# Kernel optimization log

Hardware: AMD Instinct MI355X
Metric: run time of the kernel (lower is better)

## Reference

```python
import jax, jax.numpy as jnp
import numpy as np

H = 4096        # hidden_size
I = 11008       # intermediate_size
R = 32          # low-rank error-correction rank
NLEV = 16       # int4 -> 16 levels
Q_ZERO = 7.5    # symmetric int4 zero point
Q_STEP = 0.005  # per-channel scale multiplier (keeps dequantized weights ~N(0, 1/sqrt(H)) scale)
LR_SCALE = 0.02 # low-rank correction magnitude


def setup_inputs() -> dict:
    key = jax.random.key(0)
    ks = jax.random.split(key, 13)
    B, S = 2, 2048
    inp = {
        "x": jax.random.normal(ks[0], (B, S, H), jnp.float32),
        "gate_q": jax.random.randint(ks[1], (I, H), 0, NLEV, jnp.int32),
        "gate_scale": jax.random.uniform(ks[2], (I,), jnp.float32),
        "gate_A": jax.random.normal(ks[3], (H, R), jnp.float32),
        "gate_B": jax.random.normal(ks[4], (R, I), jnp.float32),
        "up_q": jax.random.randint(ks[5], (I, H), 0, NLEV, jnp.int32),
        "up_scale": jax.random.uniform(ks[6], (I,), jnp.float32),
        "up_A": jax.random.normal(ks[7], (H, R), jnp.float32),
        "up_B": jax.random.normal(ks[8], (R, I), jnp.float32),
        "down_q": jax.random.randint(ks[9], (H, I), 0, NLEV, jnp.int32),
        "down_scale": jax.random.uniform(ks[10], (H,), jnp.float32),
        "down_A": jax.random.normal(ks[11], (I, R), jnp.float32),
        "down_B": jax.random.normal(ks[12], (R, H), jnp.float32),
    }
    return inp


def _qlinear(x, q, scale, A, Bm):
    # Dequantize int4 weight [out, in] with per-output-channel scale, then
    # y = x @ W^T + LR_SCALE * (x @ A) @ B   (LQER low-rank error correction)
    w = (q.astype(jnp.float32) - Q_ZERO) * (scale * Q_STEP)[:, None]
    y = jnp.einsum('bsh,oh->bso', x, w)
    return y + LR_SCALE * ((x @ A) @ Bm)


def reference(x, gate_q, gate_scale, gate_A, gate_B,
              up_q, up_scale, up_A, up_B,
              down_q, down_scale, down_A, down_B):
    g = _qlinear(x, gate_q, gate_scale, gate_A, gate_B)   # [B,S,I]
    u = _qlinear(x, up_q, up_scale, up_A, up_B)           # [B,S,I]
    h = jax.nn.silu(g) * u                                # SwiGLU gating
    return _qlinear(h, down_q, down_scale, down_A, down_B)  # [B,S,H]
```

## Files before the change

kernel.cpp:

```cpp
#include <hip/hip_runtime.h>
#include <hip/hip_bf16.h>
#include <stdint.h>

#define H_DIM 4096
#define I_DIM 11008
#define M_TOK 4096

typedef __attribute__((ext_vector_type(8))) short short8;
typedef __attribute__((ext_vector_type(4))) float f32x4;
typedef __attribute__((ext_vector_type(4))) int   i32x4;

#define SX_DIV 6.0f
#define QS (0.0025f * SX_DIV / 127.0f)

static __device__ __forceinline__ float bf2f(unsigned short u) {
    union { uint32_t i; float f; } v; v.i = ((uint32_t)u) << 16; return v.f;
}
static __device__ __forceinline__ unsigned short f2bf(float f) {
    union { float f; uint32_t i; } v; v.f = f;
    uint32_t r = v.i + 0x7FFF + ((v.i >> 16) & 1);
    return (unsigned short)(r >> 16);
}

static __device__ __forceinline__ void gload16(const void* g, void* l) {
    __builtin_amdgcn_global_load_lds(
        (const __attribute__((address_space(1))) void*)g,
        (__attribute__((address_space(3))) void*)l, 16, 0, 0);
}

__global__ void k_prep_all(
    const float* __restrict__ x,
    const int* __restrict__ gq, const int* __restrict__ uq,
    const float* __restrict__ gA, const float* __restrict__ uA,
    const float* __restrict__ dA,
    const float* __restrict__ gB, const float* __restrict__ uB,
    const float* __restrict__ dB,
    unsigned short* __restrict__ xbf, char* __restrict__ xi8,
    char* __restrict__ Wg8, char* __restrict__ Wu8,
    unsigned short* __restrict__ AgT, unsigned short* __restrict__ AuT,
    unsigned short* __restrict__ AdBf,
    unsigned short* __restrict__ BgT, unsigned short* __restrict__ BuT,
    unsigned short* __restrict__ BdT)
{
    const int stride = gridDim.x * blockDim.x;
    const int tid0 = blockIdx.x * blockDim.x + threadIdx.x;
    const int XN4 = (M_TOK * H_DIM) / 4;
    const float SXI = 127.0f / SX_DIV;
    for (int i = tid0; i < XN4; i += stride) {
        f32x4 v = ((const f32x4*)x)[i];
        uint64_t p = (uint64_t)f2bf(v[0]) | ((uint64_t)f2bf(v[1]) << 16) |
                     ((uint64_t)f2bf(v[2]) << 32) | ((uint64_t)f2bf(v[3]) << 48);
        ((uint64_t*)xbf)[i] = p;
        uint32_t q8 = 0;
#pragma unroll
        for (int t = 0; t < 4; t++) {
            int a = (int)lrintf(v[t] * SXI);
            a = a > 127 ? 127 : (a < -127 ? -127 : a);
            q8 |= ((uint32_t)(a & 255)) << (8 * t);
        }
        ((uint32_t*)xi8)[i] = q8;
    }
    const int QN4 = (I_DIM * H_DIM) / 4;
    for (int i = tid0; i < 2 * QN4; i += stride) {
        int j = i; const int* src; char* dst;
        if (j < QN4) { src = gq; dst = Wg8; } else { j -= QN4; src = uq; dst = Wu8; }
        i32x4 qv = ((const i32x4*)src)[j];
        uint32_t p = 0;
#pragma unroll
        for (int t = 0; t < 4; t++)
            p |= ((uint32_t)((2 * qv[t] - 15) & 255)) << (8 * t);
        ((uint32_t*)dst)[j] = p;
    }
    const int AT = 32 * H_DIM;
    for (int i = tid0; i < 2 * AT; i += stride) {
        int j = i; const float* src; unsigned short* dst;
        if (j < AT) { src = gA; dst = AgT; } else { j -= AT; src = uA; dst = AuT; }
        int r = j >> 12, k = j & 4095;
        dst[j] = f2bf(src[k * 32 + r]);
    }
    const int AD = I_DIM * 32;
    for (int i = tid0; i < AD; i += stride) AdBf[i] = f2bf(dA[i]);
    const int TBI = I_DIM * 32, TBH = H_DIM * 32;
    for (int i = tid0; i < 2 * TBI + TBH; i += stride) {
        int j = i; const float* src; unsigned short* dst; int N;
        if (j < TBI) { src = gB; dst = BgT; N = I_DIM; }
        else if ((j -= TBI) < TBI) { src = uB; dst = BuT; N = I_DIM; }
        else { j -= TBI; src = dB; dst = BdT; N = H_DIM; }
        int n = j >> 5, r = j & 31;
        dst[j] = f2bf(src[r * N + n]);
    }
}

__global__ __launch_bounds__(256) void k_T(
    const unsigned short* __restrict__ xbf,
    const unsigned short* __restrict__ AgT,
    const unsigned short* __restrict__ AuT,
    unsigned short* __restrict__ Tg,
    unsigned short* __restrict__ Tu)
{
    const unsigned short* AT = blockIdx.y ? AuT : AgT;
    unsigned short* T = blockIdx.y ? Tu : Tg;
    const int wid = threadIdx.x >> 6, lane = threadIdx.x & 63;
    const int base = blockIdx.x * 64 + wid * 16;
    const int l15 = lane & 15, kg = (lane >> 4) * 8;
    f32x4 acc0 = {}, acc1 = {};
    for (int k0 = 0; k0 < H_DIM; k0 += 32) {
        short8 af = *(const short8*)&xbf[(size_t)(base + l15) * H_DIM + k0 + kg];
        short8 b0 = *(const short8*)&AT[(size_t)l15 * H_DIM + k0 + kg];
        short8 b1 = *(const short8*)&AT[(size_t)(16 + l15) * H_DIM + k0 + kg];
        acc0 = __builtin_amdgcn_mfma_f32_16x16x32_bf16(af, b0, acc0, 0, 0, 0);
        acc1 = __builtin_amdgcn_mfma_f32_16x16x32_bf16(af, b1, acc1, 0, 0, 0);
    }
    const int q4 = lane >> 4;
#pragma unroll
    for (int t = 0; t < 4; t++) {
        int m = base + q4 * 4 + t;
        T[m * 32 + l15]      = f2bf(acc0[t] * 0.02f);
        T[m * 32 + 16 + l15] = f2bf(acc1[t] * 0.02f);
    }
}

__global__ __launch_bounds__(256) void k_wprep(
    const unsigned short* __restrict__ BT,
    const unsigned short* __restrict__ Abf,
    const int* __restrict__ q,
    const float* __restrict__ scale,
    unsigned short* __restrict__ W,
    int Nw, int Kw)
{
    __shared__ unsigned short As[128 * 32];
    __shared__ unsigned short Bs[128 * 32];
    const int tid = threadIdx.x, wid = tid >> 6, lane = tid & 63;
    const int wr = wid >> 1, wc = wid & 1;
    const int brow = blockIdx.y * 128;
    const int bcol = blockIdx.x * 128;
    const int srow = wid * 16 + (lane >> 2), scol = (lane & 3) * 8;

    gload16(BT + (size_t)(brow + srow) * 32 + scol,        &As[wid * 512]);
    gload16(BT + (size_t)(brow + 64 + srow) * 32 + scol,   &As[wid * 512 + 2048]);
    gload16(Abf + (size_t)(bcol + srow) * 32 + scol,       &Bs[wid * 512]);
    gload16(Abf + (size_t)(bcol + 64 + srow) * 32 + scol,  &Bs[wid * 512 + 2048]);
    __syncthreads();

    const int fr = lane & 15, kg = (lane >> 4) * 8;
    f32x4 acc[4][4] = {};
    short8 af[4], bfr[4];
#pragma unroll
    for (int i = 0; i < 4; i++)
        af[i] = *(const short8*)&As[(wr * 64 + i * 16 + fr) * 32 + kg];
#pragma unroll
    for (int j = 0; j < 4; j++)
        bfr[j] = *(const short8*)&Bs[(wc * 64 + j * 16 + fr) * 32 + kg];
#pragma unroll
    for (int i = 0; i < 4; i++)
#pragma unroll
        for (int j = 0; j < 4; j++)
            acc[i][j] = __builtin_amdgcn_mfma_f32_16x16x32_bf16(af[i], bfr[j], acc[i][j], 0, 0, 0);

    const int q4 = lane >> 4;
#pragma unroll
    for (int i = 0; i < 4; i++) {
#pragma unroll
        for (int t = 0; t < 4; t++) {
            int n = brow + wr * 64 + i * 16 + q4 * 4 + t;
            float sc = scale[n] * 0.005f;
#pragma unroll
            for (int j = 0; j < 4; j++) {
                int k = bcol + wc * 64 + j * 16 + fr;
                size_t off = (size_t)n * Kw + k;
                float w = ((float)q[off] - 7.5f) * sc + 0.02f * acc[i][j][t];
                W[off] = f2bf(w);
            }
        }
    }
}

__global__ __launch_bounds__(512, 1) void k_gemmfu8(
    const char* __restrict__ Xq,
    const char* __restrict__ Wg8,
    const char* __restrict__ Wu8,
    const unsigned short* __restrict__ Tg,
    const unsigned short* __restrict__ Tu,
    const unsigned short* __restrict__ BgT,
    const unsigned short* __restrict__ BuT,
    const float* __restrict__ gs, const float* __restrict__ us,
    unsigned short* __restrict__ H,
    int M, int NI, int K)
{
    extern __shared__ char dynsmem[];
    char* smem = dynsmem;
    const int tid = threadIdx.x, wid = tid >> 6, lane = tid & 63;
    const int wr = wid >> 2, wc = wid & 3;

    const int gx = NI >> 7;
    const int nwg = gx * (M >> 8);
    int orig = blockIdx.y * gx + blockIdx.x;
    int q8 = nwg >> 3, r8 = nwg & 7;
    int xcd = orig & 7, lid = orig >> 3;
    int wg = (xcd < r8 ? xcd * (q8 + 1) : r8 * (q8 + 1) + (xcd - r8) * q8) + lid;
    const int bcol = (wg % gx) << 7;
    const int brow = (wg / gx) << 8;

    const int srow = wid * 16 + (lane >> 2);
    const int scolB = ((lane & 3) ^ ((lane >> 3) & 3)) * 16;
    const char* aSrc  = Xq  + (size_t)(brow + srow) * K + scolB;
    const char* bgSrc = Wg8 + (size_t)(bcol + srow) * K + scolB;
    const char* buSrc = Wu8 + (size_t)(bcol + srow) * K + scolB;
    const int ldwB = wid * 1024;

    i32x4 acc[8][4];
#pragma unroll
    for (int i = 0; i < 8; ++i)
#pragma unroll
        for (int j = 0; j < 4; ++j) acc[i][j] = (i32x4){0, 0, 0, 0};

    i32x4 A0f[4], A1f[4], BgAf[2], BgBf[2], Buf[2];
    const int l15 = lane & 15, q4b = lane >> 4;
    const int ps = (q4b ^ ((l15 >> 1) & 3)) * 16;
    const char* aRd = smem + (wr * 64 + l15) * 64 + ps;
    const char* bRd = smem + 16384 + (wc * 32 + l15) * 64 + ps;
    const int NT = K >> 6;

#define SA0(BB, k0) gload16(aSrc + (k0), smem + (BB)*32768 + ldwB)
#define SA1(BB, k0) gload16(aSrc + 128*(size_t)K + (k0), smem + (BB)*32768 + 8192 + ldwB)
#define SBG(BB, k0) gload16(bgSrc + (k0), smem + (BB)*32768 + 16384 + ldwB)
#define SBU(BB, k0) gload16(buSrc + (k0), smem + (BB)*32768 + 24576 + ldwB)
#define LDA0(BB) { _Pragma("unroll") for (int i4 = 0; i4 < 4; ++i4) \
    A0f[i4] = *(const i32x4*)(aRd + (BB)*32768 + i4*1024); }
#define LDA1(BB) { _Pragma("unroll") for (int i4 = 0; i4 < 4; ++i4) \
    A1f[i4] = *(const i32x4*)(aRd + (BB)*32768 + 8192 + i4*1024); }
#define LDBG(SET, BB) { _Pragma("unroll") for (int j2 = 0; j2 < 2; ++j2) \
    SET[j2] = *(const i32x4*)(bRd + (BB)*32768 + j2*1024); }
#define LDBU(BB) { _Pragma("unroll") for (int j2 = 0; j2 < 2; ++j2) \
    Buf[j2] = *(const i32x4*)(bRd + (BB)*32768 + 8192 + j2*1024); }
#define MFI(AF, BF, IH, JB) { __builtin_amdgcn_s_setprio(1); \
    _Pragma("unroll") for (int i4 = 0; i4 < 4; ++i4) \
    _Pragma("unroll") for (int j2 = 0; j2 < 2; ++j2) \
        acc[(IH)*4+i4][(JB)*2+j2] = __builtin_amdgcn_mfma_i32_16x16x64_i8( \
            AF[i4], BF[j2], acc[(IH)*4+i4][(JB)*2+j2], 0, 0, 0); \
    __builtin_amdgcn_s_setprio(0); }
#define BARR() __builtin_amdgcn_s_barrier()

#define FTILE(BB, BGC, BGN, k2, S2, CERT, RN) { \
    LDBU(BB); \
    BARR(); \
    MFI(A0f, BGC, 0, 0); \
    LDA1(BB); \
    BARR(); \
    if (S2) { SA0(BB, k2); SBG(BB, k2); } \
    MFI(A0f, Buf, 0, 1); \
    if (CERT == 1) asm volatile("s_waitcnt vmcnt(2)" ::: "memory"); \
    if (CERT == 2) asm volatile("s_waitcnt vmcnt(0)" ::: "memory"); \
    BARR(); \
    if (S2) { SBU(BB, k2); } \
    MFI(A1f, Buf, 1, 1); \
    if (RN) { LDA0(1-(BB)); LDBG(BGN, 1-(BB)); } \
    BARR(); \
    if (S2) { SA1(BB, k2); } \
    MFI(A1f, BGC, 1, 0); \
}

    SA0(0, 0); SBG(0, 0); SBU(0, 0); SA1(0, 0);
    SA0(1, 64); SBG(1, 64); SBU(1, 64); SA1(1, 64);
    asm volatile("s_waitcnt vmcnt(4)" ::: "memory");
    BARR();
    LDA0(0); LDBG(BgAf, 0);

    for (int u = 0; u < (NT - 2) / 2; ++u) {
        const int k2a = (2 * u + 2) << 6, k2b = (2 * u + 3) << 6;
        FTILE(0, BgAf, BgBf, k2a, 1, 1, 1);
        FTILE(1, BgBf, BgAf, k2b, 1, 1, 1);
    }
    FTILE(0, BgAf, BgBf, 0, 0, 2, 1);
    FTILE(1, BgBf, BgAf, 0, 0, 0, 0);

#undef FTILE
#undef BARR
#undef MFI
#undef LDBU
#undef LDBG
#undef LDA1
#undef LDA0
#undef SBU
#undef SBG
#undef SA1
#undef SA0

    __builtin_amdgcn_s_barrier();
    {
        const int scolH = (lane & 3) * 8;
        gload16(Tg + (size_t)(brow + srow) * 32 + scolH,        smem + ldwB);
        gload16(Tg + (size_t)(brow + 128 + srow) * 32 + scolH,  smem + 8192 + ldwB);
        gload16(Tu + (size_t)(brow + srow) * 32 + scolH,        smem + 16384 + ldwB);
        gload16(Tu + (size_t)(brow + 128 + srow) * 32 + scolH,  smem + 24576 + ldwB);
        gload16(BgT + (size_t)(bcol + srow) * 32 + scolH,       smem + 32768 + ldwB);
        gload16(BuT + (size_t)(bcol + srow) * 32 + scolH,       smem + 40960 + ldwB);
    }
    asm volatile("s_waitcnt vmcnt(0)" ::: "memory");
    __builtin_amdgcn_s_barrier();

    const int fr = l15;
    short8 BgF[2], BuF[2];
#pragma unroll
    for (int j2 = 0; j2 < 2; ++j2) {
        BgF[j2] = *(const short8*)(smem + 32768 + (wc * 32 + j2 * 16 + l15) * 64 + q4b * 16);
        BuF[j2] = *(const short8*)(smem + 40960 + (wc * 32 + j2 * 16 + l15) * 64 + q4b * 16);
    }
    float cg[2], cu[2];
#pragma unroll
    for (int j2 = 0; j2 < 2; ++j2) {
        int n = bcol + wc * 32 + j2 * 16 + fr;
        cg[j2] = gs[n] * QS;
        cu[j2] = us[n] * QS;
    }
    const int q4 = lane >> 4;
#pragma unroll
    for (int i = 0; i < 8; ++i) {
        int trow = (i >> 2) * 128 + wr * 64 + (i & 3) * 16 + l15;
        short8 tgf = *(const short8*)(smem + trow * 64 + q4b * 16);
        short8 tuf = *(const short8*)(smem + 16384 + trow * 64 + q4b * 16);
#pragma unroll
        for (int j2 = 0; j2 < 2; ++j2) {
            f32x4 ag, au;
#pragma unroll
            for (int t = 0; t < 4; ++t) {
                ag[t] = (float)acc[i][j2][t] * cg[j2];
                au[t] = (float)acc[i][2 + j2][t] * cu[j2];
            }
            ag = __builtin_amdgcn_mfma_f32_16x16x32_bf16(tgf, BgF[j2], ag, 0, 0, 0);
            au = __builtin_amdgcn_mfma_f32_16x16x32_bf16(tuf, BuF[j2], au, 0, 0, 0);
#pragma unroll
            for (int t = 0; t < 4; ++t) {
                int m = brow + (i >> 2) * 128 + wr * 64 + (i & 3) * 16 + q4 * 4 + t;
                int n = bcol + wc * 32 + j2 * 16 + fr;
                float g = ag[t];
                float s = g / (1.0f + __expf(-g));
                H[(size_t)m * NI + n] = f2bf(s * au[t]);
            }
        }
    }
}

#define STG(p, k0, doff) gload16((p) + (k0), smem + (doff) + ldw)
#define LDA8(dst, P, IH) { _Pragma("unroll") \
    for (int i4 = 0; i4 < 4; ++i4) dst[i4] = *(const short8*)&(P)[(IH)*8192 + i4*1024]; }
#define LDB4(dst, P, JH) { _Pragma("unroll") \
    for (int j2 = 0; j2 < 2; ++j2) dst[j2] = *(const short8*)&(P)[(JH)*8192 + j2*1024]; }
#define MF8(AF, BF, IH, JH) { __builtin_amdgcn_s_setprio(1); \
    _Pragma("unroll") for (int i4 = 0; i4 < 4; ++i4) \
    _Pragma("unroll") for (int j2 = 0; j2 < 2; ++j2) \
        acc[(IH)*4+i4][(JH)*2+j2] = __builtin_amdgcn_mfma_f32_16x16x32_bf16( \
            AF[i4], BF[j2], acc[(IH)*4+i4][(JH)*2+j2], 0, 0, 0); \
    __builtin_amdgcn_s_setprio(0); }

#define TILE(BB, t, S2, SB0, CERT, RNEXT) { \
    const int kN = ((t) + 1) << 6, kN2 = ((t) + 2) << 6; \
    LDA8(afY, aP[BB][1], 0); LDB4(bfY, bP[BB][1], 0); \
    __builtin_amdgcn_s_barrier(); \
    if (SB0) { STG(bS[0], kN, (1-(BB))*32768 + 16384); \
               STG(bS[1], kN, (1-(BB))*32768 + 20480); } \
    MF8(afX, bfX, 0, 0); \
    LDB4(bfX, bP[BB][0], 1); \
    __builtin_amdgcn_s_barrier(); \
    MF8(afY, bfY, 0, 0); \
    LDB4(bfY, bP[BB][1], 1); \
    __builtin_amdgcn_s_barrier(); \
    if (S2) { STG(aS[0], kN2, (BB)*32768); STG(aS[1], kN2, (BB)*32768 + 4096); } \
    MF8(afX, bfX, 0, 1); \
    LDA8(afX, aP[BB][0], 1); \
    __builtin_amdgcn_s_barrier(); \
    MF8(afY, bfY, 0, 1); \
    LDA8(afY, aP[BB][1], 1); \
    if (CERT == 1) asm volatile("s_waitcnt vmcnt(2)" ::: "memory"); \
    if (CERT == 2) asm volatile("s_waitcnt vmcnt(0)" ::: "memory"); \
    __builtin_amdgcn_s_barrier(); \
    if (S2) { STG(bS[2], kN2, (BB)*32768 + 24576); STG(bS[3], kN2, (BB)*32768 + 28672); } \
    MF8(afX, bfX, 1, 1); \
    LDB4(bfX, bP[BB][0], 0); \
    __builtin_amdgcn_s_barrier(); \
    MF8(afY, bfY, 1, 1); \
    LDB4(bfY, bP[BB][1], 0); \
    __builtin_amdgcn_s_barrier(); \
    if (S2) { STG(aS[2], kN2, (BB)*32768 + 8192); STG(aS[3], kN2, (BB)*32768 + 12288); } \
    MF8(afX, bfX, 1, 0); \
    if (RNEXT) { LDA8(afX, aP[1-(BB)][0], 0); LDB4(bfX, bP[1-(BB)][0], 0); } \
    __builtin_amdgcn_s_barrier(); \
    MF8(afY, bfY, 1, 0); \
}

#define GEMM_BODY(K_) { \
    const int NT = (K_) >> 6; \
    STG(aS[0], 0, 0);      STG(aS[1], 0, 4096); \
    STG(bS[0], 0, 16384);  STG(bS[1], 0, 20480); \
    STG(bS[2], 0, 24576);  STG(bS[3], 0, 28672); \
    STG(aS[2], 0, 8192);   STG(aS[3], 0, 12288); \
    STG(aS[0], 64, 32768);         STG(aS[1], 64, 32768 + 4096); \
    STG(bS[2], 64, 32768 + 24576); STG(bS[3], 64, 32768 + 28672); \
    STG(aS[2], 64, 32768 + 8192);  STG(aS[3], 64, 32768 + 12288); \
    asm volatile("s_waitcnt vmcnt(6)" ::: "memory"); \
    __builtin_amdgcn_s_barrier(); \
    LDA8(afX, aP[0][0], 0); LDB4(bfX, bP[0][0], 0); \
    int t = 0; \
    for (; t + 4 <= NT; t += 2) { \
        TILE(0, t,     1, 1, 1, 1); \
        TILE(1, t + 1, 1, 1, 1, 1); \
    } \
    TILE(0, NT - 2, 0, 1, 2, 1); \
    TILE(1, NT - 1, 0, 0, 0, 0); \
}

__global__ __launch_bounds__(512, 1) void k_gemmdown(
    const unsigned short* __restrict__ A,
    const unsigned short* __restrict__ B,
    float* __restrict__ C,
    int M, int N, int K)
{
    extern __shared__ char dynsmem[];
    unsigned short* smem = (unsigned short*)dynsmem;
    const int tid = threadIdx.x, wid = tid >> 6, lane = tid & 63;
    const int wr = wid >> 2, wc = wid & 3;

    const int gx = N >> 8;
    const int nwg = gx * (M >> 8);
    int orig = blockIdx.y * gx + blockIdx.x;
    int q8 = nwg >> 3, r8 = nwg & 7;
    int xcd = orig & 7, lid = orig >> 3;
    int wg = (xcd < r8 ? xcd * (q8 + 1) : r8 * (q8 + 1) + (xcd - r8) * q8) + lid;
    const int bcol = (wg % gx) << 8;
    const int brow = (wg / gx) << 8;

    const int rg = lane >> 3;
    const int ss = ((lane & 7) ^ rg) * 8;
    const unsigned short* aS[4];
    const unsigned short* bS[4];
#pragma unroll
    for (int c = 0; c < 4; c++) {
        int row = c * 64 + wid * 8 + rg;
        aS[c] = A + (size_t)(brow + row) * K + ss;
        bS[c] = B + (size_t)(bcol + row) * K + ss;
    }
    const int ldw = wid * 512;

    f32x4 acc[8][4] = {};
    short8 afX[4], afY[4], bfX[2], bfY[2];
    const int fr = lane & 15, qk = lane >> 4, f7 = fr & 7;

    const unsigned short* aP[2][2];
    const unsigned short* bP[2][2];
#pragma unroll
    for (int b = 0; b < 2; ++b)
#pragma unroll
        for (int kk = 0; kk < 2; ++kk) {
            int swz = (((kk << 2) | qk) ^ f7) << 3;
            aP[b][kk] = smem + b * 32768 + (wr * 64 + fr) * 64 + swz;
            bP[b][kk] = smem + b * 32768 + 16384 + (wc * 32 + fr) * 64 + swz;
        }

    GEMM_BODY(K);

    const int q4 = lane >> 4;
#pragma unroll
    for (int i = 0; i < 8; ++i) {
#pragma unroll
        for (int j = 0; j < 4; ++j) {
#pragma unroll
            for (int tt = 0; tt < 4; ++tt) {
                int m = brow + (i >> 2) * 128 + wr * 64 + (i & 3) * 16 + q4 * 4 + tt;
                int n = bcol + (j >> 1) * 128 + wc * 32 + (j & 1) * 16 + fr;
                C[(size_t)m * N + n] = acc[i][j][tt];
            }
        }
    }
}

extern "C" void kernel_launch(void* const* d_in, const int* in_sizes, int n_in,
                              void* d_out, int out_size, void* d_ws, size_t ws_size,
                              hipStream_t stream) {
    (void)in_sizes; (void)n_in; (void)out_size; (void)ws_size;
    const float* x          = (const float*)d_in[0];
    const int*   gate_q     = (const int*)d_in[1];
    const float* gate_scale = (const float*)d_in[2];
    const float* gate_A     = (const float*)d_in[3];
    const float* gate_B     = (const float*)d_in[4];
    const int*   up_q       = (const int*)d_in[5];
    const float* up_scale   = (const float*)d_in[6];
    const float* up_A       = (const float*)d_in[7];
    const float* up_B       = (const float*)d_in[8];
    const int*   down_q     = (const int*)d_in[9];
    const float* down_scale = (const float*)d_in[10];
    const float* down_A     = (const float*)d_in[11];
    const float* down_B     = (const float*)d_in[12];

    char* ws = (char*)d_ws;
    size_t off = 0;
    auto alloc = [&](size_t bytes) {
        void* p = ws + off; off += (bytes + 255) & ~(size_t)255; return p;
    };
    unsigned short* xbf  = (unsigned short*)alloc((size_t)M_TOK * H_DIM * 2);
    char*           xi8  = (char*)alloc((size_t)M_TOK * H_DIM);
    char*           Wg8  = (char*)alloc((size_t)I_DIM * H_DIM);
    char*           Wu8  = (char*)alloc((size_t)I_DIM * H_DIM);
    unsigned short* wdm  = (unsigned short*)alloc((size_t)H_DIM * I_DIM * 2);
    unsigned short* hbuf = (unsigned short*)alloc((size_t)M_TOK * I_DIM * 2);
    unsigned short* Tg   = (unsigned short*)alloc((size_t)M_TOK * 32 * 2);
    unsigned short* Tu   = (unsigned short*)alloc((size_t)M_TOK * 32 * 2);
    unsigned short* AgT  = (unsigned short*)alloc((size_t)32 * H_DIM * 2);
    unsigned short* AuT  = (unsigned short*)alloc((size_t)32 * H_DIM * 2);
    unsigned short* AdBf = (unsigned short*)alloc((size_t)I_DIM * 32 * 2);
    unsigned short* BgT  = (unsigned short*)alloc((size_t)I_DIM * 32 * 2);
    unsigned short* BuT  = (unsigned short*)alloc((size_t)I_DIM * 32 * 2);
    unsigned short* BdT  = (unsigned short*)alloc((size_t)H_DIM * 32 * 2);

    (void)hipFuncSetAttribute((const void*)k_gemmfu8,
        hipFuncAttributeMaxDynamicSharedMemorySize, 65536);
    (void)hipFuncSetAttribute((const void*)k_gemmdown,
        hipFuncAttributeMaxDynamicSharedMemorySize, 131072);

    k_prep_all<<<2048, 256, 0, stream>>>(x, gate_q, up_q, gate_A, up_A, down_A,
                                         gate_B, up_B, down_B,
                                         xbf, xi8, Wg8, Wu8, AgT, AuT, AdBf,
                                         BgT, BuT, BdT);

    k_T<<<dim3(M_TOK / 64, 2), 256, 0, stream>>>(xbf, AgT, AuT, Tg, Tu);

    k_wprep<<<dim3(I_DIM / 128, H_DIM / 128), 256, 0, stream>>>(
        BdT, AdBf, down_q, down_scale, wdm, H_DIM, I_DIM);

    k_gemmfu8<<<dim3(I_DIM / 128, M_TOK / 256), 512, 65536, stream>>>(
        xi8, Wg8, Wu8, Tg, Tu, BgT, BuT, gate_scale, up_scale,
        hbuf, M_TOK, I_DIM, H_DIM);

    k_gemmdown<<<dim3(H_DIM / 256, M_TOK / 256), 512, 131072, stream>>>(
        hbuf, wdm, (float*)d_out, M_TOK, H_DIM, I_DIM);
}
```

Baseline: 898.0 us.

## Quantize down projection to int8 MFMA with separate low-rank correction

The down projection moves from a bf16 GEMM over a dequantized weight that folds in the low-rank term to an int8 x int8 GEMM. The gate/up kernel now also writes an int8-quantized copy of h using a fixed clamp range. The LQER term is computed separately as T = h@A and applied in the epilogue with a small bf16 MFMA. This removes the k_wprep weight materialization and halves operand bytes in the largest GEMM, at the cost of an extra k_T pass and accuracy risk, since h values beyond the fixed range are clipped.

Result: slower. 969.1 us (+7.9%).

```diff
diff --git a/kernel.cpp b/kernel.cpp
--- a/kernel.cpp
+++ b/kernel.cpp
@@ -11,7 +11,9 @@
 typedef __attribute__((ext_vector_type(4))) int   i32x4;
 
 #define SX_DIV 6.0f
-#define QS (0.0025f * SX_DIV / 127.0f)
+#define QS  (0.0025f * SX_DIV / 127.0f)
+#define SH_MAX 768.0f
+#define QSD (0.0025f * SH_MAX / 127.0f)
 
 static __device__ __forceinline__ float bf2f(unsigned short u) {
     union { uint32_t i; float f; } v; v.i = ((uint32_t)u) << 16; return v.f;
@@ -31,14 +33,15 @@
 __global__ void k_prep_all(
     const float* __restrict__ x,
     const int* __restrict__ gq, const int* __restrict__ uq,
+    const int* __restrict__ dq,
     const float* __restrict__ gA, const float* __restrict__ uA,
     const float* __restrict__ dA,
     const float* __restrict__ gB, const float* __restrict__ uB,
     const float* __restrict__ dB,
     unsigned short* __restrict__ xbf, char* __restrict__ xi8,
-    char* __restrict__ Wg8, char* __restrict__ Wu8,
+    char* __restrict__ Wg8, char* __restrict__ Wu8, char* __restrict__ Wd8,
     unsigned short* __restrict__ AgT, unsigned short* __restrict__ AuT,
-    unsigned short* __restrict__ AdBf,
+    unsigned short* __restrict__ AdT,
     unsigned short* __restrict__ BgT, unsigned short* __restrict__ BuT,
     unsigned short* __restrict__ BdT)
 {
@@ -61,9 +64,11 @@
         ((uint32_t*)xi8)[i] = q8;
     }
     const int QN4 = (I_DIM * H_DIM) / 4;
-    for (int i = tid0; i < 2 * QN4; i += stride) {
+    for (int i = tid0; i < 3 * QN4; i += stride) {
         int j = i; const int* src; char* dst;
-        if (j < QN4) { src = gq; dst = Wg8; } else { j -= QN4; src = uq; dst = Wu8; }
+        if (j < QN4) { src = gq; dst = Wg8; }
+        else if ((j -= QN4) < QN4) { src = uq; dst = Wu8; }
+        else { j -= QN4; src = dq; dst = Wd8; }
         i32x4 qv = ((const i32x4*)src)[j];
         uint32_t p = 0;
 #pragma unroll
@@ -78,8 +83,11 @@
         int r = j >> 12, k = j & 4095;
         dst[j] = f2bf(src[k * 32 + r]);
     }
-    const int AD = I_DIM * 32;
-    for (int i = tid0; i < AD; i += stride) AdBf[i] = f2bf(dA[i]);
+    const int ATD = 32 * I_DIM;
+    for (int i = tid0; i < ATD; i += stride) {
+        int r = i / I_DIM, k = i - r * I_DIM;
+        AdT[i] = f2bf(dA[k * 32 + r]);
+    }
     const int TBI = I_DIM * 32, TBH = H_DIM * 32;
     for (int i = tid0; i < 2 * TBI + TBH; i += stride) {
         int j = i; const float* src; unsigned short* dst; int N;
@@ -92,22 +100,19 @@
 }
 
 __global__ __launch_bounds__(256) void k_T(
-    const unsigned short* __restrict__ xbf,
-    const unsigned short* __restrict__ AgT,
-    const unsigned short* __restrict__ AuT,
-    unsigned short* __restrict__ Tg,
-    unsigned short* __restrict__ Tu)
+    const unsigned short* __restrict__ in,
+    const unsigned short* __restrict__ AT,
+    unsigned short* __restrict__ T,
+    int K)
 {
-    const unsigned short* AT = blockIdx.y ? AuT : AgT;
-    unsigned short* T = blockIdx.y ? Tu : Tg;
     const int wid = threadIdx.x >> 6, lane = threadIdx.x & 63;
     const int base = blockIdx.x * 64 + wid * 16;
     const int l15 = lane & 15, kg = (lane >> 4) * 8;
     f32x4 acc0 = {}, acc1 = {};
-    for (int k0 = 0; k0 < H_DIM; k0 += 32) {
-        short8 af = *(const short8*)&xbf[(size_t)(base + l15) * H_DIM + k0 + kg];
-        short8 b0 = *(const short8*)&AT[(size_t)l15 * H_DIM + k0 + kg];
-        short8 b1 = *(const short8*)&AT[(size_t)(16 + l15) * H_DIM + k0 + kg];
+    for (int k0 = 0; k0 < K; k0 += 32) {
+        short8 af = *(const short8*)&in[(size_t)(base + l15) * K + k0 + kg];
+        short8 b0 = *(const short8*)&AT[(size_t)l15 * K + k0 + kg];
+        short8 b1 = *(const short8*)&AT[(size_t)(16 + l15) * K + k0 + kg];
         acc0 = __builtin_amdgcn_mfma_f32_16x16x32_bf16(af, b0, acc0, 0, 0, 0);
         acc1 = __builtin_amdgcn_mfma_f32_16x16x32_bf16(af, b1, acc1, 0, 0, 0);
     }
@@ -117,61 +122,6 @@
         int m = base + q4 * 4 + t;
         T[m * 32 + l15]      = f2bf(acc0[t] * 0.02f);
         T[m * 32 + 16 + l15] = f2bf(acc1[t] * 0.02f);
-    }
-}
-
-__global__ __launch_bounds__(256) void k_wprep(
-    const unsigned short* __restrict__ BT,
-    const unsigned short* __restrict__ Abf,
-    const int* __restrict__ q,
-    const float* __restrict__ scale,
-    unsigned short* __restrict__ W,
-    int Nw, int Kw)
-{
-    __shared__ unsigned short As[128 * 32];
-    __shared__ unsigned short Bs[128 * 32];
-    const int tid = threadIdx.x, wid = tid >> 6, lane = tid & 63;
-    const int wr = wid >> 1, wc = wid & 1;
-    const int brow = blockIdx.y * 128;
-    const int bcol = blockIdx.x * 128;
-    const int srow = wid * 16 + (lane >> 2), scol = (lane & 3) * 8;
-
-    gload16(BT + (size_t)(brow + srow) * 32 + scol,        &As[wid * 512]);
-    gload16(BT + (size_t)(brow + 64 + srow) * 32 + scol,   &As[wid * 512 + 2048]);
-    gload16(Abf + (size_t)(bcol + srow) * 32 + scol,       &Bs[wid * 512]);
-    gload16(Abf + (size_t)(bcol + 64 + srow) * 32 + scol,  &Bs[wid * 512 + 2048]);
-    __syncthreads();
-
-    const int fr = lane & 15, kg = (lane >> 4) * 8;
-    f32x4 acc[4][4] = {};
-    short8 af[4], bfr[4];
-#pragma unroll
-    for (int i = 0; i < 4; i++)
-        af[i] = *(const short8*)&As[(wr * 64 + i * 16 + fr) * 32 + kg];
-#pragma unroll
-    for (int j = 0; j < 4; j++)
-        bfr[j] = *(const short8*)&Bs[(wc * 64 + j * 16 + fr) * 32 + kg];
-#pragma unroll
-    for (int i = 0; i < 4; i++)
-#pragma unroll
-        for (int j = 0; j < 4; j++)
-            acc[i][j] = __builtin_amdgcn_mfma_f32_16x16x32_bf16(af[i], bfr[j], acc[i][j], 0, 0, 0);
-
-    const int q4 = lane >> 4;
-#pragma unroll
-    for (int i = 0; i < 4; i++) {
-#pragma unroll
-        for (int t = 0; t < 4; t++) {
-            int n = brow + wr * 64 + i * 16 + q4 * 4 + t;
-            float sc = scale[n] * 0.005f;
-#pragma unroll
-            for (int j = 0; j < 4; j++) {
-                int k = bcol + wc * 64 + j * 16 + fr;
-                size_t off = (size_t)n * Kw + k;
-                float w = ((float)q[off] - 7.5f) * sc + 0.02f * acc[i][j][t];
-                W[off] = f2bf(w);
-            }
-        }
     }
 }
 
@@ -185,6 +135,7 @@
     const unsigned short* __restrict__ BuT,
     const float* __restrict__ gs, const float* __restrict__ us,
     unsigned short* __restrict__ H,
+    char* __restrict__ Hq,
     int M, int NI, int K)
 {
     extern __shared__ char dynsmem[];
@@ -314,6 +265,7 @@
         cu[j2] = us[n] * QS;
     }
     const int q4 = lane >> 4;
+    const float HSI = 127.0f / SH_MAX;
 #pragma unroll
     for (int i = 0; i < 8; ++i) {
         int trow = (i >> 2) * 128 + wr * 64 + (i & 3) * 16 + l15;
@@ -335,88 +287,27 @@
                 int n = bcol + wc * 32 + j2 * 16 + fr;
                 float g = ag[t];
                 float s = g / (1.0f + __expf(-g));
-                H[(size_t)m * NI + n] = f2bf(s * au[t]);
+                float h = s * au[t];
+                H[(size_t)m * NI + n] = f2bf(h);
+                int a = (int)lrintf(h * HSI);
+                a = a > 127 ? 127 : (a < -127 ? -127 : a);
+                Hq[(size_t)m * NI + n] = (char)a;
             }
         }
     }
 }
 
-#define STG(p, k0, doff) gload16((p) + (k0), smem + (doff) + ldw)
-#define LDA8(dst, P, IH) { _Pragma("unroll") \
-    for (int i4 = 0; i4 < 4; ++i4) dst[i4] = *(const short8*)&(P)[(IH)*8192 + i4*1024]; }
-#define LDB4(dst, P, JH) { _Pragma("unroll") \
-    for (int j2 = 0; j2 < 2; ++j2) dst[j2] = *(const short8*)&(P)[(JH)*8192 + j2*1024]; }
-#define MF8(AF, BF, IH, JH) { __builtin_amdgcn_s_setprio(1); \
-    _Pragma("unroll") for (int i4 = 0; i4 < 4; ++i4) \
-    _Pragma("unroll") for (int j2 = 0; j2 < 2; ++j2) \
-        acc[(IH)*4+i4][(JH)*2+j2] = __builtin_amdgcn_mfma_f32_16x16x32_bf16( \
-            AF[i4], BF[j2], acc[(IH)*4+i4][(JH)*2+j2], 0, 0, 0); \
-    __builtin_amdgcn_s_setprio(0); }
-
-#define TILE(BB, t, S2, SB0, CERT, RNEXT) { \
-    const int kN = ((t) + 1) << 6, kN2 = ((t) + 2) << 6; \
-    LDA8(afY, aP[BB][1], 0); LDB4(bfY, bP[BB][1], 0); \
-    __builtin_amdgcn_s_barrier(); \
-    if (SB0) { STG(bS[0], kN, (1-(BB))*32768 + 16384); \
-               STG(bS[1], kN, (1-(BB))*32768 + 20480); } \
-    MF8(afX, bfX, 0, 0); \
-    LDB4(bfX, bP[BB][0], 1); \
-    __builtin_amdgcn_s_barrier(); \
-    MF8(afY, bfY, 0, 0); \
-    LDB4(bfY, bP[BB][1], 1); \
-    __builtin_amdgcn_s_barrier(); \
-    if (S2) { STG(aS[0], kN2, (BB)*32768); STG(aS[1], kN2, (BB)*32768 + 4096); } \
-    MF8(afX, bfX, 0, 1); \
-    LDA8(afX, aP[BB][0], 1); \
-    __builtin_amdgcn_s_barrier(); \
-    MF8(afY, bfY, 0, 1); \
-    LDA8(afY, aP[BB][1], 1); \
-    if (CERT == 1) asm volatile("s_waitcnt vmcnt(2)" ::: "memory"); \
-    if (CERT == 2) asm volatile("s_waitcnt vmcnt(0)" ::: "memory"); \
-    __builtin_amdgcn_s_barrier(); \
-    if (S2) { STG(bS[2], kN2, (BB)*32768 + 24576); STG(bS[3], kN2, (BB)*32768 + 28672); } \
-    MF8(afX, bfX, 1, 1); \
-    LDB4(bfX, bP[BB][0], 0); \
-    __builtin_amdgcn_s_barrier(); \
-    MF8(afY, bfY, 1, 1); \
-    LDB4(bfY, bP[BB][1], 0); \
-    __builtin_amdgcn_s_barrier(); \
-    if (S2) { STG(aS[2], kN2, (BB)*32768 + 8192); STG(aS[3], kN2, (BB)*32768 + 12288); } \
-    MF8(afX, bfX, 1, 0); \
-    if (RNEXT) { LDA8(afX, aP[1-(BB)][0], 0); LDB4(bfX, bP[1-(BB)][0], 0); } \
-    __builtin_amdgcn_s_barrier(); \
-    MF8(afY, bfY, 1, 0); \
-}
-
-#define GEMM_BODY(K_) { \
-    const int NT = (K_) >> 6; \
-    STG(aS[0], 0, 0);      STG(aS[1], 0, 4096); \
-    STG(bS[0], 0, 16384);  STG(bS[1], 0, 20480); \
-    STG(bS[2], 0, 24576);  STG(bS[3], 0, 28672); \
-    STG(aS[2], 0, 8192);   STG(aS[3], 0, 12288); \
-    STG(aS[0], 64, 32768);         STG(aS[1], 64, 32768 + 4096); \
-    STG(bS[2], 64, 32768 + 24576); STG(bS[3], 64, 32768 + 28672); \
-    STG(aS[2], 64, 32768 + 8192);  STG(aS[3], 64, 32768 + 12288); \
-    asm volatile("s_waitcnt vmcnt(6)" ::: "memory"); \
-    __builtin_amdgcn_s_barrier(); \
-    LDA8(afX, aP[0][0], 0); LDB4(bfX, bP[0][0], 0); \
-    int t = 0; \
-    for (; t + 4 <= NT; t += 2) { \
-        TILE(0, t,     1, 1, 1, 1); \
-        TILE(1, t + 1, 1, 1, 1, 1); \
-    } \
-    TILE(0, NT - 2, 0, 1, 2, 1); \
-    TILE(1, NT - 1, 0, 0, 0, 0); \
-}
-
-__global__ __launch_bounds__(512, 1) void k_gemmdown(
-    const unsigned short* __restrict__ A,
-    const unsigned short* __restrict__ B,
+__global__ __launch_bounds__(512, 1) void k_gemmd8(
+    const char* __restrict__ Hq,
+    const char* __restrict__ Wd8,
+    const unsigned short* __restrict__ Td,
+    const unsigned short* __restrict__ BdT,
+    const float* __restrict__ ds,
     float* __restrict__ C,
     int M, int N, int K)
 {
     extern __shared__ char dynsmem[];
-    unsigned short* smem = (unsigned short*)dynsmem;
+    char* smem = dynsmem;
     const int tid = threadIdx.x, wid = tid >> 6, lane = tid & 63;
     const int wr = wid >> 2, wc = wid & 3;
 
@@ -429,45 +320,137 @@
     const int bcol = (wg % gx) << 8;
     const int brow = (wg / gx) << 8;
 
-    const int rg = lane >> 3;
-    const int ss = ((lane & 7) ^ rg) * 8;
-    const unsigned short* aS[4];
-    const unsigned short* bS[4];
-#pragma unroll
-    for (int c = 0; c < 4; c++) {
-        int row = c * 64 + wid * 8 + rg;
-        aS[c] = A + (size_t)(brow + row) * K + ss;
-        bS[c] = B + (size_t)(bcol + row) * K + ss;
-    }
-    const int ldw = wid * 512;
-
-    f32x4 acc[8][4] = {};
-    short8 afX[4], afY[4], bfX[2], bfY[2];
-    const int fr = lane & 15, qk = lane >> 4, f7 = fr & 7;
-
-    const unsigned short* aP[2][2];
-    const unsigned short* bP[2][2];
-#pragma unroll
-    for (int b = 0; b < 2; ++b)
-#pragma unroll
-        for (int kk = 0; kk < 2; ++kk) {
-            int swz = (((kk << 2) | qk) ^ f7) << 3;
-            aP[b][kk] = smem + b * 32768 + (wr * 64 + fr) * 64 + swz;
-            bP[b][kk] = smem + b * 32768 + 16384 + (wc * 32 + fr) * 64 + swz;
-        }
-
-    GEMM_BODY(K);
-
+    const int srow = wid * 16 + (lane >> 2);
+    const int scolB = ((lane & 3) ^ ((lane >> 3) & 3)) * 16;
+    const char* aSrc  = Hq  + (size_t)(brow + srow) * K + scolB;
+    const char* bgSrc = Wd8 + (size_t)(bcol + srow) * K + scolB;
+    const char* buSrc = Wd8 + (size_t)(bcol + 128 + srow) * K + scolB;
+    const int ldwB = wid * 1024;
+
+    i32x4 acc[8][4];
+#pragma unroll
+    for (int i = 0; i < 8; ++i)
+#pragma unroll
+        for (int j = 0; j < 4; ++j) acc[i][j] = (i32x4){0, 0, 0, 0};
+
+    i32x4 A0f[4], A1f[4], BgAf[2], BgBf[2], Buf[2];
+    const int l15 = lane & 15, q4b = lane >> 4;
+    const int ps = (q4b ^ ((l15 >> 1) & 3)) * 16;
+    const char* aRd = smem + (wr * 64 + l15) * 64 + ps;
+    const char* bRd = smem + 16384 + (wc * 32 + l15) * 64 + ps;
+    const int NT = K >> 6;
+
+#define SA0(BB, k0) gload16(aSrc + (k0), smem + (BB)*32768 + ldwB)
+#define SA1(BB, k0) gload16(aSrc + 128*(size_t)K + (k0), smem + (BB)*32768 + 8192 + ldwB)
+#define SBG(BB, k0) gload16(bgSrc + (k0), smem + (BB)*32768 + 16384 + ldwB)
+#define SBU(BB, k0) gload16(buSrc + (k0), smem + (BB)*32768 + 24576 + ldwB)
+#define LDA0(BB) { _Pragma("unroll") for (int i4 = 0; i4 < 4; ++i4) \
+    A0f[i4] = *(const i32x4*)(aRd + (BB)*32768 + i4*1024); }
+#define LDA1(BB) { _Pragma("unroll") for (int i4 = 0; i4 < 4; ++i4) \
+    A1f[i4] = *(const i32x4*)(aRd + (BB)*32768 + 8192 + i4*1024); }
+#define LDBG(SET, BB) { _Pragma("unroll") for (int j2 = 0; j2 < 2; ++j2) \
+    SET[j2] = *(const i32x4*)(bRd + (BB)*32768 + j2*1024); }
+#define LDBU(BB) { _Pragma("unroll") for (int j2 = 0; j2 < 2; ++j2) \
+    Buf[j2] = *(const i32x4*)(bRd + (BB)*32768 + 8192 + j2*1024); }
+#define MFI(AF, BF, IH, JB) { __builtin_amdgcn_s_setprio(1); \
+    _Pragma("unroll") for (int i4 = 0; i4 < 4; ++i4) \
+    _Pragma("unroll") for (int j2 = 0; j2 < 2; ++j2) \
+        acc[(IH)*4+i4][(JB)*2+j2] = __builtin_amdgcn_mfma_i32_16x16x64_i8( \
+            AF[i4], BF[j2], acc[(IH)*4+i4][(JB)*2+j2], 0, 0, 0); \
+    __builtin_amdgcn_s_setprio(0); }
+#define BARR() __builtin_amdgcn_s_barrier()
+
+#define FTILE(BB, BGC, BGN, k2, S2, CERT, RN) { \
+    LDBU(BB); \
+    BARR(); \
+    MFI(A0f, BGC, 0, 0); \
+    LDA1(BB); \
+    BARR(); \
+    if (S2) { SA0(BB, k2); SBG(BB, k2); } \
+    MFI(A0f, Buf, 0, 1); \
+    if (CERT == 1) asm volatile("s_waitcnt vmcnt(2)" ::: "memory"); \
+    if (CERT == 2) asm volatile("s_waitcnt vmcnt(0)" ::: "memory"); \
+    BARR(); \
+    if (S2) { SBU(BB, k2); } \
+    MFI(A1f, Buf, 1, 1); \
+    if (RN) { LDA0(1-(BB)); LDBG(BGN, 1-(BB)); } \
+    BARR(); \
+    if (S2) { SA1(BB, k2); } \
+    MFI(A1f, BGC, 1, 0); \
+}
+
+    SA0(0, 0); SBG(0, 0); SBU(0, 0); SA1(0, 0);
+    SA0(1, 64); SBG(1, 64); SBU(1, 64); SA1(1, 64);
+    asm volatile("s_waitcnt vmcnt(4)" ::: "memory");
+    BARR();
+    LDA0(0); LDBG(BgAf, 0);
+
+    for (int u = 0; u < (NT - 2) / 2; ++u) {
+        const int k2a = (2 * u + 2) << 6, k2b = (2 * u + 3) << 6;
+        FTILE(0, BgAf, BgBf, k2a, 1, 1, 1);
+        FTILE(1, BgBf, BgAf, k2b, 1, 1, 1);
+    }
+    FTILE(0, BgAf, BgBf, 0, 0, 2, 1);
+    FTILE(1, BgBf, BgAf, 0, 0, 0, 0);
+
+#undef FTILE
+#undef BARR
+#undef MFI
+#undef LDBU
+#undef LDBG
+#undef LDA1
+#undef LDA0
+#undef SBU
+#undef SBG
+#undef SA1
+#undef SA0
+
+    __builtin_amdgcn_s_barrier();
+    {
+        const int scolH = (lane & 3) * 8;
+        gload16(Td + (size_t)(brow + srow) * 32 + scolH,         smem + ldwB);
+        gload16(Td + (size_t)(brow + 128 + srow) * 32 + scolH,   smem + 8192 + ldwB);
+        gload16(BdT + (size_t)(bcol + srow) * 32 + scolH,        smem + 16384 + ldwB);
+        gload16(BdT + (size_t)(bcol + 128 + srow) * 32 + scolH,  smem + 24576 + ldwB);
+    }
+    asm volatile("s_waitcnt vmcnt(0)" ::: "memory");
+    __builtin_amdgcn_s_barrier();
+
+    const int fr = l15;
+    short8 Bd0[2], Bd1[2];
+#pragma unroll
+    for (int j2 = 0; j2 < 2; ++j2) {
+        Bd0[j2] = *(const short8*)(smem + 16384 + (wc * 32 + j2 * 16 + l15) * 64 + q4b * 16);
+        Bd1[j2] = *(const short8*)(smem + 24576 + (wc * 32 + j2 * 16 + l15) * 64 + q4b * 16);
+    }
+    float c0[2], c1[2];
+#pragma unroll
+    for (int j2 = 0; j2 < 2; ++j2) {
+        int n0 = bcol + wc * 32 + j2 * 16 + fr;
+        c0[j2] = ds[n0] * QSD;
+        c1[j2] = ds[n0 + 128] * QSD;
+    }
     const int q4 = lane >> 4;
 #pragma unroll
     for (int i = 0; i < 8; ++i) {
-#pragma unroll
-        for (int j = 0; j < 4; ++j) {
-#pragma unroll
-            for (int tt = 0; tt < 4; ++tt) {
-                int m = brow + (i >> 2) * 128 + wr * 64 + (i & 3) * 16 + q4 * 4 + tt;
-                int n = bcol + (j >> 1) * 128 + wc * 32 + (j & 1) * 16 + fr;
-                C[(size_t)m * N + n] = acc[i][j][tt];
+        int trow = (i >> 2) * 128 + wr * 64 + (i & 3) * 16 + l15;
+        short8 tdf = *(const short8*)(smem + trow * 64 + q4b * 16);
+#pragma unroll
+        for (int j2 = 0; j2 < 2; ++j2) {
+            f32x4 a0, a1;
+#pragma unroll
+            for (int t = 0; t < 4; ++t) {
+                a0[t] = (float)acc[i][j2][t] * c0[j2];
+                a1[t] = (float)acc[i][2 + j2][t] * c1[j2];
+            }
+            a0 = __builtin_amdgcn_mfma_f32_16x16x32_bf16(tdf, Bd0[j2], a0, 0, 0, 0);
+            a1 = __builtin_amdgcn_mfma_f32_16x16x32_bf16(tdf, Bd1[j2], a1, 0, 0, 0);
+#pragma unroll
+            for (int t = 0; t < 4; ++t) {
+                int m = brow + (i >> 2) * 128 + wr * 64 + (i & 3) * 16 + q4 * 4 + t;
+                int n = bcol + wc * 32 + j2 * 16 + fr;
+                C[(size_t)m * N + n] = a0[t];
+                C[(size_t)m * N + n + 128] = a1[t];
             }
         }
     }
@@ -500,36 +483,39 @@
     char*           xi8  = (char*)alloc((size_t)M_TOK * H_DIM);
     char*           Wg8  = (char*)alloc((size_t)I_DIM * H_DIM);
     char*           Wu8  = (char*)alloc((size_t)I_DIM * H_DIM);
-    unsigned short* wdm  = (unsigned short*)alloc((size_t)H_DIM * I_DIM * 2);
+    char*           Wd8  = (char*)alloc((size_t)H_DIM * I_DIM);
     unsigned short* hbuf = (unsigned short*)alloc((size_t)M_TOK * I_DIM * 2);
+    char*           hq   = (char*)alloc((size_t)M_TOK * I_DIM);
     unsigned short* Tg   = (unsigned short*)alloc((size_t)M_TOK * 32 * 2);
     unsigned short* Tu   = (unsigned short*)alloc((size_t)M_TOK * 32 * 2);
+    unsigned short* Td   = (unsigned short*)alloc((size_t)M_TOK * 32 * 2);
     unsigned short* AgT  = (unsigned short*)alloc((size_t)32 * H_DIM * 2);
     unsigned short* AuT  = (unsigned short*)alloc((size_t)32 * H_DIM * 2);
-    unsigned short* AdBf = (unsigned short*)alloc((size_t)I_DIM * 32 * 2);
+    unsigned short* AdT  = (unsigned short*)alloc((size_t)32 * I_DIM * 2);
     unsigned short* BgT  = (unsigned short*)alloc((size_t)I_DIM * 32 * 2);
     unsigned short* BuT  = (unsigned short*)alloc((size_t)I_DIM * 32 * 2);
     unsigned short* BdT  = (unsigned short*)alloc((size_t)H_DIM * 32 * 2);
 
     (void)hipFuncSetAttribute((const void*)k_gemmfu8,
         hipFuncAttributeMaxDynamicSharedMemorySize, 65536);
-    (void)hipFuncSetAttribute((const void*)k_gemmdown,
-        hipFuncAttributeMaxDynamicSharedMemorySize, 131072);
-
-    k_prep_all<<<2048, 256, 0, stream>>>(x, gate_q, up_q, gate_A, up_A, down_A,
+    (void)hipFuncSetAttribute((const void*)k_gemmd8,
+        hipFuncAttributeMaxDynamicSharedMemorySize, 65536);
+
+    k_prep_all<<<2048, 256, 0, stream>>>(x, gate_q, up_q, down_q,
+                                         gate_A, up_A, down_A,
                                          gate_B, up_B, down_B,
-                                         xbf, xi8, Wg8, Wu8, AgT, AuT, AdBf,
+                                         xbf, xi8, Wg8, Wu8, Wd8, AgT, AuT, AdT,
                                          BgT, BuT, BdT);
 
-    k_T<<<dim3(M_TOK / 64, 2), 256, 0, stream>>>(xbf, AgT, AuT, Tg, Tu);
-
-    k_wprep<<<dim3(I_DIM / 128, H_DIM / 128), 256, 0, stream>>>(
-        BdT, AdBf, down_q, down_scale, wdm, H_DIM, I_DIM);
+    k_T<<<M_TOK / 64, 256, 0, stream>>>(xbf, AgT, Tg, H_DIM);
+    k_T<<<M_TOK / 64, 256, 0, stream>>>(xbf, AuT, Tu, H_DIM);
 
     k_gemmfu8<<<dim3(I_DIM / 128, M_TOK / 256), 512, 65536, stream>>>(
         xi8, Wg8, Wu8, Tg, Tu, BgT, BuT, gate_scale, up_scale,
-        hbuf, M_TOK, I_DIM, H_DIM);
-
-    k_gemmdown<<<dim3(H_DIM / 256, M_TOK / 256), 512, 131072, stream>>>(
-        hbuf, wdm, (float*)d_out, M_TOK, H_DIM, I_DIM);
-}
+        hbuf, hq, M_TOK, I_DIM, H_DIM);
+
+    k_T<<<M_TOK / 64, 256, 0, stream>>>(hbuf, AdT, Td, I_DIM);
+
+    k_gemmd8<<<dim3(H_DIM / 256, M_TOK / 256), 512, 65536, stream>>>(
+        hq, Wd8, Td, BdT, down_scale, (float*)d_out, M_TOK, H_DIM, I_DIM);
+}
```
